# Optimization experiments

Hardware: AMD Instinct MI355X
Metric: run time of the kernel (lower is better)

The kernel has to match this reference:

```python
import jax, jax.numpy as jnp
import numpy as np

D = 256; H = 4; HD = 64; WBAND = 64; KLOC = 8; EMAK = 256
SUMDECAY = 0.9; STATEDECAY = 0.9; STEP = 0.5


def _dwconv(x, kern, pad):
    # x: (B,T,D), kern: (D,1,K) cross-correlation taps, causal left pad
    lhs = jnp.transpose(x, (0, 2, 1))
    out = jax.lax.conv_general_dilated(
        lhs, kern, (1,), [(pad, 0)],
        dimension_numbers=('NCH', 'OIH', 'NCH'),
        feature_group_count=x.shape[-1])
    return jnp.transpose(out, (0, 2, 1))


def _ln(x, g, b):
    m = jnp.mean(x, -1, keepdims=True)
    v = jnp.var(x, -1, keepdims=True)
    return (x - m) * jax.lax.rsqrt(v + 1e-5) * g + b


def _lin(x, w, b):
    return jnp.dot(x, w.T) + b


def _forward(parallel_repr, sequential_state, trajectory_summary, conv_w, conv_b,
             qkv_w, qkv_b, mo_w, mo_b, fg_w, fg_b, gkv_w, gkv_b, go_w, go_b,
             comb_w, comb_b, ffn1_w, ffn1_b, ffn2_w, ffn2_b, tr1_w, tr1_b,
             tr2_w, tr2_b, p2s_w, p2s_b, s2p_w, s2p_b,
             ln1_g, ln1_b, ln2_g, ln2_b, ln3_g, ln3_b, ln4_g, ln4_b):
    B, T, _ = parallel_repr.shape
    # Tier 1: local depthwise causal conv (window 8); torch pads both sides then slices [:T] == causal left pad
    local_history = _dwconv(parallel_repr, conv_w, KLOC - 1) + conv_b
    # Tier 2: banded causal attention (keep j in [i-63, i])
    qkv = _lin(parallel_repr, qkv_w, qkv_b).reshape(B, T, 3, H, HD)
    qkv = jnp.transpose(qkv, (2, 0, 3, 1, 4))  # (3,B,H,T,HD)
    q, k, v = qkv[0], qkv[1], qkv[2]
    idx = jnp.arange(T)
    band = (idx[:, None] >= idx[None, :]) & (idx[None, :] > idx[:, None] - WBAND)
    scores = jnp.einsum('bhqd,bhkd->bhqk', q, k) / jnp.sqrt(jnp.float32(HD))
    attn = jax.nn.softmax(jnp.where(band, scores, -1e9), -1)
    med = jnp.einsum('bhqk,bhkd->bhqd', attn, v)
    med = jnp.transpose(med, (0, 2, 1, 3)).reshape(B, T, D)
    med = _lin(med, mo_w, mo_b)
    fg = jax.nn.sigmoid(_lin(jnp.concatenate([parallel_repr, med], -1), fg_w, fg_b))
    medium_out = med * fg
    # Tier 3: causal cumulative (linear-attention style) global concepts
    gkv = _lin(parallel_repr, gkv_w, gkv_b)
    gk, gv = jnp.split(gkv, 2, -1)
    gk = jax.nn.elu(gk) + 1.0
    concepts = jnp.cumsum(gk * gv, 1) / (jnp.cumsum(gk, 1) + 1e-5)
    global_out = _lin(concepts, go_w, go_b)
    combined = _lin(jnp.concatenate([local_history, medium_out, global_out], -1), comb_w, comb_b)
    pr = _ln(parallel_repr + combined, ln1_g, ln1_b)
    # EMA summary via 256-tap causal depthwise conv: w[i] = (1-d)*d^i
    kE = min(T, EMAK)
    taps = (1.0 - SUMDECAY) * SUMDECAY ** jnp.arange(kE, dtype=jnp.float32)
    kern = jnp.broadcast_to(taps[::-1][None, None, :], (D, 1, kE))
    global_summary = _dwconv(pr, kern, kE - 1)
    guidance = _lin(pr, p2s_w, p2s_b)
    cs = jnp.concatenate([pr + 0.3 * guidance, global_summary], -1)
    deltas = jnp.tanh(_lin(jax.nn.gelu(_lin(cs, tr1_w, tr1_b), approximate=False), tr2_w, tr2_b))
    scaled = deltas * STEP
    # state accumulation via conv trick: acc[t] = sum_i d^i * delta[t-i]
    staps = STATEDECAY ** jnp.arange(kE, dtype=jnp.float32)
    skern = jnp.broadcast_to(staps[::-1][None, None, :], (D, 1, kE))
    acc = _dwconv(scaled, skern, kE - 1)
    dpow = STATEDECAY ** jnp.arange(1, T + 1, dtype=jnp.float32)
    pre_ln = sequential_state[:, None, :] * dpow[None, :, None] + acc
    states = _ln(pre_ln, ln3_g, ln3_b)
    seq_g = _lin(states, s2p_w, s2p_b)
    ffn = _lin(jax.nn.gelu(_lin(pr + 0.3 * seq_g, ffn1_w, ffn1_b), approximate=False), ffn2_w, ffn2_b)
    pr_out = _ln(pr + ffn, ln2_g, ln2_b)
    final_state = _ln(states[:, -1, :], ln4_g, ln4_b)
    final_traj = global_summary[:, -1, :]
    return pr_out, final_state, final_traj


def setup_inputs():
    key = jax.random.key(0)
    ks = jax.random.split(key, 20)
    B, T = 4, 2048
    s = 0.02
    def w(i, shape):
        return jax.random.normal(ks[i], shape, jnp.float32) * s
    return {
        'parallel_repr': jax.random.normal(ks[0], (B, T, D), jnp.float32),
        'sequential_state': jax.random.normal(ks[1], (B, D), jnp.float32),
        'trajectory_summary': jax.random.normal(ks[2], (B, D), jnp.float32),
        'conv_w': w(3, (D, 1, KLOC)), 'conv_b': jnp.zeros((D,)),
        'qkv_w': w(4, (3 * D, D)), 'qkv_b': jnp.zeros((3 * D,)),
        'mo_w': w(5, (D, D)), 'mo_b': jnp.zeros((D,)),
        'fg_w': w(6, (D, 2 * D)), 'fg_b': jnp.zeros((D,)),
        'gkv_w': w(7, (2 * D, D)), 'gkv_b': jnp.zeros((2 * D,)),
        'go_w': w(8, (D, D)), 'go_b': jnp.zeros((D,)),
        'comb_w': w(9, (D, 3 * D)), 'comb_b': jnp.zeros((D,)),
        'ffn1_w': w(10, (4 * D, D)), 'ffn1_b': jnp.zeros((4 * D,)),
        'ffn2_w': w(11, (D, 4 * D)), 'ffn2_b': jnp.zeros((D,)),
        'tr1_w': w(12, (2 * D, 2 * D)), 'tr1_b': jnp.zeros((2 * D,)),
        'tr2_w': w(13, (D, 2 * D)), 'tr2_b': jnp.zeros((D,)),
        'p2s_w': w(14, (D, D)), 'p2s_b': jnp.zeros((D,)),
        's2p_w': w(15, (D, D)), 's2p_b': jnp.zeros((D,)),
        'ln1_g': jnp.ones((D,)), 'ln1_b': jnp.zeros((D,)),
        'ln2_g': jnp.ones((D,)), 'ln2_b': jnp.zeros((D,)),
        'ln3_g': jnp.ones((D,)), 'ln3_b': jnp.zeros((D,)),
        'ln4_g': jnp.ones((D,)), 'ln4_b': jnp.zeros((D,)),
    }


def reference(parallel_repr, sequential_state, trajectory_summary, conv_w, conv_b,
              qkv_w, qkv_b, mo_w, mo_b, fg_w, fg_b, gkv_w, gkv_b, go_w, go_b,
              comb_w, comb_b, ffn1_w, ffn1_b, ffn2_w, ffn2_b, tr1_w, tr1_b,
              tr2_w, tr2_b, p2s_w, p2s_b, s2p_w, s2p_b,
              ln1_g, ln1_b, ln2_g, ln2_b, ln3_g, ln3_b, ln4_g, ln4_b):
    return _forward(parallel_repr, sequential_state, trajectory_summary, conv_w, conv_b,
                    qkv_w, qkv_b, mo_w, mo_b, fg_w, fg_b, gkv_w, gkv_b, go_w, go_b,
                    comb_w, comb_b, ffn1_w, ffn1_b, ffn2_w, ffn2_b, tr1_w, tr1_b,
                    tr2_w, tr2_b, p2s_w, p2s_b, s2p_w, s2p_b,
                    ln1_g, ln1_b, ln2_g, ln2_b, ln3_g, ln3_b, ln4_g, ln4_b)
```

## Files before the change

kernel.cpp:

```cpp
#include <hip/hip_runtime.h>
#include <hip/hip_bf16.h>
#include <math.h>

#define D_  256
#define T_  2048
#define B_  4
#define M_  (B_*T_)
#define H_  4
#define HD_ 64

#define NC_ 64
#define LCH (T_/NC_)

enum { OP_NONE=0, OP_SIGMUL=1, OP_ADDAUX=2, OP_AXPBY=3, OP_GELU=4, OP_TANHHALF=5 };

typedef unsigned short u16;
typedef short short8 __attribute__((ext_vector_type(8)));
typedef float f32x4  __attribute__((ext_vector_type(4)));

__device__ __forceinline__ float gelu_f(float x){ return 0.5f*x*(1.0f+erff(x*0.70710678118654752f)); }
__device__ __forceinline__ float sigmoid_f(float x){ return 1.0f/(1.0f+expf(-x)); }

__device__ __forceinline__ unsigned pk2(float a, float b){
    __hip_bfloat162 h = __float22bfloat162_rn(make_float2(a,b));
    union { __hip_bfloat162 h; unsigned u; } c; c.h = h; return c.u;
}
__device__ __forceinline__ float bfu(u16 u){ return __uint_as_float(((unsigned)u)<<16); }
__device__ __forceinline__ u16 bf1(float x){ return (u16)(pk2(x,x)&0xffffu); }

#define OFF_QKV   0u
#define OFF_MO    327680u
#define OFF_FG    393216u
#define OFF_GO    524288u
#define OFF_COMB  589824u
#define OFF_FFN1  786432u
#define OFF_FFN2  1048576u
#define OFF_TR1   1310720u
#define OFF_TR2   1572864u
#define OFF_P2S   1703936u
#define OFF_S2P   1769472u
#define NWELEM    1835008u
#define NXELEM    2097152u

__global__ __launch_bounds__(256) void cvt_k(
    const float* __restrict__ qkv_w, const float* __restrict__ gkv_w,
    const float* __restrict__ qkv_b, const float* __restrict__ gkv_b,
    const float* __restrict__ mo_w,  const float* __restrict__ fg_w,
    const float* __restrict__ go_w,  const float* __restrict__ comb_w,
    const float* __restrict__ ffn1_w,const float* __restrict__ ffn2_w,
    const float* __restrict__ tr1_w, const float* __restrict__ tr2_w,
    const float* __restrict__ p2s_w, const float* __restrict__ s2p_w,
    const float* __restrict__ X,
    u16* __restrict__ Wh, u16* __restrict__ Xh, float* __restrict__ bq)
{
    size_t i = ((size_t)blockIdx.x*256 + threadIdx.x)*4;
    if (i < NWELEM){
        const float* s; size_t base;
        if      (i < OFF_MO)  { s=(i<196608)?qkv_w:gkv_w; base=(i<196608)?0:196608; }
        else if (i < OFF_FG)  { s=mo_w;   base=OFF_MO; }
        else if (i < OFF_GO)  { s=fg_w;   base=OFF_FG; }
        else if (i < OFF_COMB){ s=go_w;   base=OFF_GO; }
        else if (i < OFF_FFN1){ s=comb_w; base=OFF_COMB; }
        else if (i < OFF_FFN2){ s=ffn1_w; base=OFF_FFN1; }
        else if (i < OFF_TR1) { s=ffn2_w; base=OFF_FFN2; }
        else if (i < OFF_TR2) { s=tr1_w;  base=OFF_TR1; }
        else if (i < OFF_P2S) { s=tr2_w;  base=OFF_TR2; }
        else if (i < OFF_S2P) { s=p2s_w;  base=OFF_P2S; }
        else                  { s=s2p_w;  base=OFF_S2P; }
        float4 v = *(const float4*)(s + (i-base));
        *(uint2*)(Wh + i) = (uint2){ pk2(v.x,v.y), pk2(v.z,v.w) };
    } else if (i < NWELEM + NXELEM){
        size_t j = i - NWELEM;
        float4 v = *(const float4*)(X + j);
        *(uint2*)(Xh + j) = (uint2){ pk2(v.x,v.y), pk2(v.z,v.w) };
    } else if (i < NWELEM + NXELEM + 1280){
        size_t j = i - (NWELEM + NXELEM);
        #pragma unroll
        for (int k=0;k<4;++k){
            size_t e = j + k;
            bq[e] = (e < 768) ? qkv_b[e] : gkv_b[e-768];
        }
    }
}

__global__ __launch_bounds__(512) void gemm_k(
    const u16* __restrict__ A0, const u16* __restrict__ W0, int ldw0, int K0,
    const u16* __restrict__ A1, const u16* __restrict__ W1, int ldw1, int K1,
    const u16* __restrict__ A2, const u16* __restrict__ W2, int ldw2, int K2,
    const float* __restrict__ bias, const void* __restrict__ aux, int aux_bf16,
    void* __restrict__ C, int ldc, int c_bf16, int op, int ncol)
{
    __shared__ u16 As[128*64];
    __shared__ u16 Ws[64*64];

    const int q8   = gridDim.x >> 3;
    const int lid  = (blockIdx.x & 7)*q8 + (blockIdx.x >> 3);
    const int brow = lid / ncol;
    const int bcol = lid - brow*ncol;
    const int row0 = brow*128, col0 = bcol*64;

    const int tid  = threadIdx.x;
    const int lane = tid & 63, wid = tid >> 6;
    const int wm = (wid >> 1)*32, wn = (wid & 1)*32;
    const int l15 = lane & 15, l4 = lane >> 4;
    const int rowA = tid >> 2;
    const int scA  = (tid & 3) * 8;
    const int rowW = tid >> 3;
    const int scW  = (tid & 7) * 8;

    f32x4 acc[2][2];
    #pragma unroll
    for (int i=0;i<2;++i)
        #pragma unroll
        for (int j=0;j<2;++j) acc[i][j] = (f32x4){0.f,0.f,0.f,0.f};

    uint4 ra0, ra1, rw0;

    auto loadtile = [&](const u16* A, const u16* W, int ldw, int K, int kb){
        const u16* ga = A + (size_t)(row0+rowA)*K + kb + scA;
        ra0 = *(const uint4*)ga;
        ra1 = *(const uint4*)(ga + 32);
        rw0 = *(const uint4*)(W + (size_t)(col0+rowW)*ldw + kb + scW);
    };
    auto storetile = [&](){
        const int sw = (rowA&7)<<3;
        *(uint4*)&As[(rowA*64 + scA) ^ sw]      = ra0;
        *(uint4*)&As[(rowA*64 + scA + 32) ^ sw] = ra1;
        *(uint4*)&Ws[(rowW*64 + scW) ^ ((rowW&7)<<3)] = rw0;
    };
    auto mfma_tile = [&](){
        #pragma unroll
        for (int ks=0;ks<2;++ks){
            const int koff = ks*32 + l4*8;
            short8 af[2], bf[2];
            #pragma unroll
            for (int f=0;f<2;++f){
                const int ar = wm + f*16 + l15;
                af[f] = *(const short8*)&As[(ar*64 + koff) ^ ((ar&7)<<3)];
                const int brn = wn + f*16 + l15;
                bf[f] = *(const short8*)&Ws[(brn*64 + koff) ^ ((brn&7)<<3)];
            }
            #pragma unroll
            for (int fm=0;fm<2;++fm)
                #pragma unroll
                for (int fn=0;fn<2;++fn)
                    acc[fm][fn] = __builtin_amdgcn_mfma_f32_16x16x32_bf16(
                        af[fm], bf[fn], acc[fm][fn], 0, 0, 0);
        }
    };

    const u16* Ac = A0; const u16* Wc = W0; int ldwc = ldw0, Kc = K0, kb = 0;
    loadtile(Ac, Wc, ldwc, Kc, 0);
    while (true){
        __syncthreads();
        storetile();
        __syncthreads();
        int nkb = kb + 64;
        const u16* nA = Ac; const u16* nW = Wc; int nld = ldwc, nK = Kc;
        bool have_next = true;
        if (nkb >= Kc){
            if (Ac == A0 && A1){ nA = A1; nW = W1; nld = ldw1; nK = K1; nkb = 0; }
            else if (Ac == A1 && A2){ nA = A2; nW = W2; nld = ldw2; nK = K2; nkb = 0; }
            else have_next = false;
        }
        if (have_next) loadtile(nA, nW, nld, nK, nkb);
        mfma_tile();
        if (!have_next) break;
        Ac = nA; Wc = nW; ldwc = nld; Kc = nK; kb = nkb;
    }

    #pragma unroll
    for (int fn=0;fn<2;++fn){
        const int n = col0 + wn + fn*16 + l15;
        const float bv = bias[n];
        #pragma unroll
        for (int fm=0;fm<2;++fm){
            #pragma unroll
            for (int j=0;j<4;++j){
                const int m = row0 + wm + fm*16 + l4*4 + j;
                float v = acc[fm][fn][j] + bv;
                if (op==OP_GELU)          v = gelu_f(v);
                else if (op==OP_TANHHALF) v = 0.5f*tanhf(v);
                else if (op!=OP_NONE){
                    const size_t ai = (size_t)m*D_ + n;
                    const float a = aux_bf16 ? bfu(((const u16*)aux)[ai])
                                             : ((const float*)aux)[ai];
                    if (op==OP_SIGMUL)      v = a*sigmoid_f(v);
                    else if (op==OP_ADDAUX) v = v + a;
                    else                    v = a + 0.3f*v;
                }
                if (c_bf16) ((u16*)C)[(size_t)m*ldc + n] = bf1(v);
                else        ((float*)C)[(size_t)m*ldc + n] = v;
            }
        }
    }
}

__global__ __launch_bounds__(256) void conv_k(const u16* __restrict__ Xh,
    const float* __restrict__ w, const float* __restrict__ bias, u16* __restrict__ out)
{
    int idx = blockIdx.x*256 + threadIdx.x;
    int d4 = (idx & 63) * 4;
    int bt = idx >> 6;
    int t = bt & (T_-1);
    float a0 = bias[d4], a1 = bias[d4+1], a2 = bias[d4+2], a3 = bias[d4+3];
    const u16* xp = Xh + (size_t)bt*D_ + d4;
    #pragma unroll
    for (int j=0;j<8;++j){
        int tt = t - 7 + j;
        if (tt >= 0){
            uint2 v = *(const uint2*)(xp + (size_t)(j-7)*D_);
            a0 += bfu((u16)(v.x & 0xffff))      * w[(d4+0)*8 + j];
            a1 += bfu((u16)(v.x >> 16))         * w[(d4+1)*8 + j];
            a2 += bfu((u16)(v.y & 0xffff))      * w[(d4+2)*8 + j];
            a3 += bfu((u16)(v.y >> 16))         * w[(d4+3)*8 + j];
        }
    }
    *(uint2*)(out + (size_t)bt*D_ + d4) = (uint2){ pk2(a0,a1), pk2(a2,a3) };
}

__global__ __launch_bounds__(256) void attn_k(const u16* __restrict__ QKVG,
    u16* __restrict__ MED)
{
    __shared__ u16 Kl[128*64];
    __shared__ u16 Ql[64*64];
    __shared__ u16 Vl[64*128];
    const int b = blockIdx.z, h = blockIdx.y;
    const int t0 = blockIdx.x * 64;
    const int kb0 = t0 - 64;
    const int tid = threadIdx.x;

    {
        const int r0 = tid >> 3, c8 = (tid & 7) * 8;
        #pragma unroll
        for (int rep=0;rep<4;++rep){
            const int r = r0 + rep*32;
            const int kg = kb0 + r;
            uint4 pk = {0,0,0,0}, pv = {0,0,0,0};
            if (kg >= 0){
                const u16* gp = QKVG + ((size_t)(b*T_ + kg))*1280 + h*HD_ + c8;
                pk = *(const uint4*)(gp + 256);
                pv = *(const uint4*)(gp + 512);
            }
            *(uint4*)&Kl[(r*64 + c8) ^ ((r&7)<<3)] = pk;
            const u16* pvu = (const u16*)&pv;
            #pragma unroll
            for (int j=0;j<8;++j){
                const int d = c8 + j;
                Vl[(d*128 + r) ^ ((d&15)<<3)] = pvu[j];
            }
        }
        #pragma unroll
        for (int rep=0;rep<2;++rep){
            const int r = r0 + rep*32;
            uint4 pq = *(const uint4*)(QKVG + ((size_t)(b*T_ + t0 + r))*1280 + h*HD_ + c8);
            *(uint4*)&Ql[(r*64 + c8) ^ ((r&7)<<3)] = pq;
        }
    }
    __syncthreads();

    const int lane = tid & 63, w = tid >> 6;
    const int l15 = lane & 15, l4 = lane >> 4;

    short8 bq[2];
    {
        const int qr = w*16 + l15;
        bq[0] = *(const short8*)&Ql[(qr*64 +      l4*8) ^ ((qr&7)<<3)];
        bq[1] = *(const short8*)&Ql[(qr*64 + 32 + l4*8) ^ ((qr&7)<<3)];
    }

    f32x4 s[8];
    #pragma unroll
    for (int kf=0;kf<8;++kf){
        const int kr = kf*16 + l15;
        short8 a0 = *(const short8*)&Kl[(kr*64 +      l4*8) ^ ((kr&7)<<3)];
        short8 a1 = *(const short8*)&Kl[(kr*64 + 32 + l4*8) ^ ((kr&7)<<3)];
        f32x4 acc = (f32x4){0.f,0.f,0.f,0.f};
        acc = __builtin_amdgcn_mfma_f32_16x16x32_bf16(a0, bq[0], acc, 0,0,0);
        acc = __builtin_amdgcn_mfma_f32_16x16x32_bf16(a1, bq[1], acc, 0,0,0);
        s[kf] = acc;
    }

    const int qg = t0 + w*16 + l15;
    float m = -1e30f;
    #pragma unroll
    for (int kf=0;kf<8;++kf){
        #pragma unroll
        for (int j=0;j<4;++j){
            const int kg = kb0 + kf*16 + l4*4 + j;
            const int diff = qg - kg;
            const float v = (kg >= 0 && diff >= 0 && diff < 64) ? s[kf][j]*0.125f : -1e30f;
            s[kf][j] = v;
            m = fmaxf(m, v);
        }
    }
    m = fmaxf(m, __shfl_xor(m,16));
    m = fmaxf(m, __shfl_xor(m,32));
    float lsum = 0.f;
    unsigned lo[8], hi[8];
    #pragma unroll
    for (int kf=0;kf<8;++kf){
        const float p0 = expf(s[kf][0]-m), p1 = expf(s[kf][1]-m);
        const float p2 = expf(s[kf][2]-m), p3 = expf(s[kf][3]-m);
        lsum += (p0+p1)+(p2+p3);
        lo[kf] = pk2(p0,p1);
        hi[kf] = pk2(p2,p3);
    }
    lsum += __shfl_xor(lsum,16);
    lsum += __shfl_xor(lsum,32);
    const float inv = 1.f/lsum;

    f32x4 o[4];
    #pragma unroll
    for (int df=0;df<4;++df) o[df] = (f32x4){0.f,0.f,0.f,0.f};
    const int baseLane = l15 + ((l4&1)<<5);
    const bool hiHalf = (l4>>1) != 0;
    #pragma unroll
    for (int kb=0;kb<4;++kb){
        const int x0 = __shfl((int)lo[2*kb],   baseLane);
        const int x1 = __shfl((int)hi[2*kb],   baseLane);
        const int x2 = __shfl((int)lo[2*kb],   baseLane+16);
        const int x3 = __shfl((int)hi[2*kb],   baseLane+16);
        const int y0 = __shfl((int)lo[2*kb+1], baseLane);
        const int y1 = __shfl((int)hi[2*kb+1], baseLane);
        const int y2 = __shfl((int)lo[2*kb+1], baseLane+16);
        const int y3 = __shfl((int)hi[2*kb+1], baseLane+16);
        int4 afi;
        afi.x = hiHalf ? y0 : x0;
        afi.y = hiHalf ? y1 : x1;
        afi.z = hiHalf ? y2 : x2;
        afi.w = hiHalf ? y3 : x3;
        union { int4 i; short8 s; } cv; cv.i = afi;
        #pragma unroll
        for (int df=0;df<4;++df){
            const int vr = df*16 + l15;
            short8 bv = *(const short8*)&Vl[(vr*128 + kb*32 + l4*8) ^ ((vr&15)<<3)];
            o[df] = __builtin_amdgcn_mfma_f32_16x16x32_bf16(cv.s, bv, o[df], 0,0,0);
        }
    }

    #pragma unroll
    for (int j=0;j<4;++j){
        const float invj = __shfl(inv, l4*4 + j);
        const int mrow = b*T_ + t0 + w*16 + l4*4 + j;
        u16* op = MED + (size_t)mrow*D_ + h*HD_ + l15;
        #pragma unroll
        for (int df=0;df<4;++df)
            op[df*16] = bf1(o[df][j] * invj);
    }
}

__global__ __launch_bounds__(256) void scan1_p1(const u16* __restrict__ QKVG,
    float* __restrict__ CA, float* __restrict__ CC)
{
    const int d = threadIdx.x, c = blockIdx.x, b = blockIdx.y;
    const u16* base = QKVG + ((size_t)(b*T_ + c*LCH))*1280;
    float sgk=0.f, sgkv=0.f;
    for (int t=0;t<LCH;++t){
        float gk = bfu(base[(size_t)t*1280 + 768 + d]);
        gk = gk > 0.f ? gk + 1.f : expf(gk);
        float gv = bfu(base[(size_t)t*1280 + 1024 + d]);
        sgk += gk; sgkv += gk*gv;
    }
    CA[((size_t)b*NC_ + c)*D_ + d] = sgk;
    CC[((size_t)b*NC_ + c)*D_ + d] = sgkv;
}

__global__ __launch_bounds__(256) void scan1_p3(const u16* __restrict__ QKVG,
    const float* __restrict__ CA, const float* __restrict__ CC, u16* __restrict__ CONC)
{
    const int d = threadIdx.x, c = blockIdx.x, b = blockIdx.y;
    float sgk = 0.f, sgkv = 0.f;
    for (int cc=0; cc<c; ++cc){
        sgk  += CA[((size_t)b*NC_ + cc)*D_ + d];
        sgkv += CC[((size_t)b*NC_ + cc)*D_ + d];
    }
    const u16* base = QKVG + ((size_t)(b*T_ + c*LCH))*1280;
    u16* out = CONC + ((size_t)(b*T_ + c*LCH))*D_ + d;
    for (int t=0;t<LCH;++t){
        float gk = bfu(base[(size_t)t*1280 + 768 + d]);
        gk = gk > 0.f ? gk + 1.f : expf(gk);
        float gv = bfu(base[(size_t)t*1280 + 1024 + d]);
        sgk += gk; sgkv += gk*gv;
        out[(size_t)t*D_] = bf1(sgkv / (sgk + 1e-5f));
    }
}

__global__ __launch_bounds__(256) void ema_p1h(const u16* __restrict__ X,
    float* __restrict__ CARRY, float alpha)
{
    const int d = threadIdx.x, c = blockIdx.x, b = blockIdx.y;
    const u16* xp = X + ((size_t)(b*T_ + c*LCH))*D_ + d;
    float g = 0.f;
    for (int t=0;t<LCH;++t) g = 0.9f*g + alpha*bfu(xp[(size_t)t*D_]);
    CARRY[((size_t)b*NC_ + c)*D_ + d] = g;
}

__global__ __launch_bounds__(256) void ema_p3h(const u16* __restrict__ X,
    const float* __restrict__ CARRY, u16* __restrict__ OUT, float alpha,
    float* __restrict__ traj)
{
    const int d = threadIdx.x, c = blockIdx.x, b = blockIdx.y;
    const float dL = powf(0.9f, (float)LCH);
    float g = 0.f;
    for (int cc=0; cc<c; ++cc) g = CARRY[((size_t)b*NC_ + cc)*D_ + d] + dL*g;
    const u16* xp = X + ((size_t)(b*T_ + c*LCH))*D_ + d;
    u16* op = OUT + ((size_t)(b*T_ + c*LCH))*D_ + d;
    for (int t=0;t<LCH;++t){
        g = 0.9f*g + alpha*bfu(xp[(size_t)t*D_]);
        op[(size_t)t*D_] = bf1(g);
    }
    if (c == NC_-1) traj[b*D_ + d] = g;
}

__global__ __launch_bounds__(256) void ema_p3_state_h(const u16* __restrict__ X,
    const float* __restrict__ CARRY, const float* __restrict__ SEQ, float* __restrict__ OUT)
{
    const int d = threadIdx.x, c = blockIdx.x, b = blockIdx.y;
    const float dL = powf(0.9f, (float)LCH);
    float a = 0.f;
    for (int cc=0; cc<c; ++cc) a = CARRY[((size_t)b*NC_ + cc)*D_ + d] + dL*a;
    const float ss = SEQ[b*D_ + d];
    float dp = powf(0.9f, (float)(c*LCH + 1));
    const u16* xp = X + ((size_t)(b*T_ + c*LCH))*D_ + d;
    float* op = OUT + ((size_t)(b*T_ + c*LCH))*D_ + d;
    for (int t=0;t<LCH;++t){
        a = 0.9f*a + bfu(xp[(size_t)t*D_]);
        op[(size_t)t*D_] = fmaf(ss, dp, a);
        dp *= 0.9f;
    }
}

__global__ __launch_bounds__(256) void ln_k(const float* __restrict__ in,
    const float* __restrict__ g, const float* __restrict__ b,
    float* __restrict__ out, u16* __restrict__ out2)
{
    int row  = blockIdx.x*4 + (threadIdx.x>>6);
    int lane = threadIdx.x & 63;
    const float* ip = in + (size_t)row*D_ + lane*4;
    float4 x = *(const float4*)ip;
    float s  = x.x+x.y+x.z+x.w;
    float s2 = x.x*x.x + x.y*x.y + x.z*x.z + x.w*x.w;
    #pragma unroll
    for (int o=1;o<64;o<<=1){ s += __shfl_xor(s,o); s2 += __shfl_xor(s2,o); }
    float mean = s * (1.f/256.f);
    float var  = s2 * (1.f/256.f) - mean*mean;
    float rs = rsqrtf(var + 1e-5f);
    int db = lane*4;
    float4 r;
    r.x=(x.x-mean)*rs*g[db+0]+b[db+0];
    r.y=(x.y-mean)*rs*g[db+1]+b[db+1];
    r.z=(x.z-mean)*rs*g[db+2]+b[db+2];
    r.w=(x.w-mean)*rs*g[db+3]+b[db+3];
    if (out)
        *(float4*)(out + (size_t)row*D_ + db) = r;
    if (out2)
        *(uint2*)(out2 + (size_t)row*D_ + db) = (uint2){ pk2(r.x,r.y), pk2(r.z,r.w) };
}

__global__ __launch_bounds__(256) void ln3_k(const float* __restrict__ in,
    const float* __restrict__ g3, const float* __restrict__ b3, u16* __restrict__ states,
    const float* __restrict__ g4, const float* __restrict__ b4, float* __restrict__ fsout)
{
    int row  = blockIdx.x*4 + (threadIdx.x>>6);
    int lane = threadIdx.x & 63;
    const float* ip = in + (size_t)row*D_ + lane*4;
    float4 x = *(const float4*)ip;
    float s  = x.x+x.y+x.z+x.w;
    float s2 = x.x*x.x + x.y*x.y + x.z*x.z + x.w*x.w;
    #pragma unroll
    for (int o=1;o<64;o<<=1){ s += __shfl_xor(s,o); s2 += __shfl_xor(s2,o); }
    float mean = s * (1.f/256.f);
    float var  = s2 * (1.f/256.f) - mean*mean;
    float rs = rsqrtf(var + 1e-5f);
    int db = lane*4;
    float4 st;
    st.x=(x.x-mean)*rs*g3[db+0]+b3[db+0];
    st.y=(x.y-mean)*rs*g3[db+1]+b3[db+1];
    st.z=(x.z-mean)*rs*g3[db+2]+b3[db+2];
    st.w=(x.w-mean)*rs*g3[db+3]+b3[db+3];
    *(uint2*)(states + (size_t)row*D_ + db) = (uint2){ pk2(st.x,st.y), pk2(st.z,st.w) };

    if ((row & (T_-1)) == T_-1){
        float u  = st.x+st.y+st.z+st.w;
        float u2 = st.x*st.x + st.y*st.y + st.z*st.z + st.w*st.w;
        #pragma unroll
        for (int o=1;o<64;o<<=1){ u += __shfl_xor(u,o); u2 += __shfl_xor(u2,o); }
        float m2 = u * (1.f/256.f);
        float v2 = u2 * (1.f/256.f) - m2*m2;
        float r2 = rsqrtf(v2 + 1e-5f);
        float4 fs;
        fs.x=(st.x-m2)*r2*g4[db+0]+b4[db+0];
        fs.y=(st.y-m2)*r2*g4[db+1]+b4[db+1];
        fs.z=(st.z-m2)*r2*g4[db+2]+b4[db+2];
        fs.w=(st.w-m2)*r2*g4[db+3]+b4[db+3];
        *(float4*)(fsout + (size_t)(row>>11)*D_ + db) = fs;
    }
}

extern "C" void kernel_launch(void* const* d_in, const int* in_sizes, int n_in,
                              void* d_out, int out_size, void* d_ws, size_t ws_size,
                              hipStream_t stream)
{
    const float* X     = (const float*)d_in[0];
    const float* SEQ   = (const float*)d_in[1];
    const float* conv_w= (const float*)d_in[3];
    const float* conv_b= (const float*)d_in[4];
    const float* qkv_w = (const float*)d_in[5];
    const float* qkv_b = (const float*)d_in[6];
    const float* mo_w  = (const float*)d_in[7];
    const float* mo_b  = (const float*)d_in[8];
    const float* fg_w  = (const float*)d_in[9];
    const float* fg_b  = (const float*)d_in[10];
    const float* gkv_w = (const float*)d_in[11];
    const float* gkv_b = (const float*)d_in[12];
    const float* go_w  = (const float*)d_in[13];
    const float* go_b  = (const float*)d_in[14];
    const float* comb_w= (const float*)d_in[15];
    const float* comb_b= (const float*)d_in[16];
    const float* ffn1_w= (const float*)d_in[17];
    const float* ffn1_b= (const float*)d_in[18];
    const float* ffn2_w= (const float*)d_in[19];
    const float* ffn2_b= (const float*)d_in[20];
    const float* tr1_w = (const float*)d_in[21];
    const float* tr1_b = (const float*)d_in[22];
    const float* tr2_w = (const float*)d_in[23];
    const float* tr2_b = (const float*)d_in[24];
    const float* p2s_w = (const float*)d_in[25];
    const float* p2s_b = (const float*)d_in[26];
    const float* s2p_w = (const float*)d_in[27];
    const float* s2p_b = (const float*)d_in[28];
    const float* ln1_g = (const float*)d_in[29];
    const float* ln1_b = (const float*)d_in[30];
    const float* ln2_g = (const float*)d_in[31];
    const float* ln2_b = (const float*)d_in[32];
    const float* ln3_g = (const float*)d_in[33];
    const float* ln3_b = (const float*)d_in[34];
    const float* ln4_g = (const float*)d_in[35];
    const float* ln4_b = (const float*)d_in[36];

    char* p = (char*)d_ws;
    auto alloc = [&](size_t bytes)->char*{ char* r = p; p += (bytes + 255) & ~(size_t)255; return r; };

    u16*   QKVG = (u16*)  alloc((size_t)M_*1280*2);
    u16*   Wh   = (u16*)  alloc((size_t)NWELEM*2);
    float* bq   = (float*)alloc(1280*4);
    u16*   Xh   = (u16*)  alloc((size_t)M_*256*2);
    u16*   MED  = (u16*)  alloc((size_t)M_*256*2);
    u16*   MED2 = (u16*)  alloc((size_t)M_*256*2);
    u16*   LH   = (u16*)  alloc((size_t)M_*256*2);
    u16*   CONC = (u16*)  alloc((size_t)M_*256*2);
    u16*   GOUT = (u16*)  alloc((size_t)M_*256*2);
    u16*   MOUT = (u16*)  alloc((size_t)M_*256*2);
    float* PRE1 = (float*)alloc((size_t)M_*256*4);
    u16*   PRh  = (u16*)  alloc((size_t)M_*256*2);
    u16*   GSUM = (u16*)  alloc((size_t)M_*256*2);
    u16*   CS1  = (u16*)  alloc((size_t)M_*256*2);
    u16*   H1   = (u16*)  alloc((size_t)M_*512*2);
    u16*   SCALEDh=(u16*) alloc((size_t)M_*256*2);
    float* PRE3 = (float*)alloc((size_t)M_*256*4);
    u16*   STATESh=(u16*) alloc((size_t)M_*256*2);
    u16*   FFNIN= (u16*)  alloc((size_t)M_*256*2);
    u16*   H2   = (u16*)  alloc((size_t)M_*1024*2);
    float* PRE2 = (float*)alloc((size_t)M_*256*4);
    float* CAR0 = (float*)alloc((size_t)B_*NC_*D_*4);
    float* CAR1 = (float*)alloc((size_t)B_*NC_*D_*4);

    float* out_pr = (float*)d_out;
    float* out_fs = out_pr + (size_t)M_*256;
    float* out_tj = out_fs + B_*256;

    const dim3 blk256(256), blk512(512);
    const dim3 scan_grid(NC_, B_);
    const int NRg = M_/128;

    cvt_k<<<dim3(3842), blk256, 0, stream>>>(
        qkv_w, gkv_w, qkv_b, gkv_b, mo_w, fg_w, go_w, comb_w,
        ffn1_w, ffn2_w, tr1_w, tr2_w, p2s_w, s2p_w, X, Wh, Xh, bq);
    gemm_k<<<dim3(NRg*20), blk512, 0, stream>>>(
        Xh, Wh+OFF_QKV, 256, 256,  nullptr,nullptr,0,0,  nullptr,nullptr,0,0,
        bq, nullptr, 0, QKVG, 1280, 1, OP_NONE, 20);
    conv_k<<<dim3(M_*D_/1024), blk256, 0, stream>>>(Xh, conv_w, conv_b, LH);
    attn_k<<<dim3(T_/64, H_, B_), blk256, 0, stream>>>(QKVG, MED);
    gemm_k<<<dim3(NRg*4), blk512, 0, stream>>>(
        MED, Wh+OFF_MO, 256, 256,  nullptr,nullptr,0,0,  nullptr,nullptr,0,0,
        mo_b, nullptr, 0, MED2, 256, 1, OP_NONE, 4);
    scan1_p1<<<scan_grid, blk256, 0, stream>>>(QKVG, CAR0, CAR1);
    scan1_p3<<<scan_grid, blk256, 0, stream>>>(QKVG, CAR0, CAR1, CONC);
    gemm_k<<<dim3(NRg*4), blk512, 0, stream>>>(
        CONC, Wh+OFF_GO, 256, 256,  nullptr,nullptr,0,0,  nullptr,nullptr,0,0,
        go_b, nullptr, 0, GOUT, 256, 1, OP_NONE, 4);
    gemm_k<<<dim3(NRg*4), blk512, 0, stream>>>(
        Xh, Wh+OFF_FG, 512, 256,  MED2, Wh+OFF_FG+256, 512, 256,  nullptr,nullptr,0,0,
        fg_b, MED2, 1, MOUT, 256, 1, OP_SIGMUL, 4);
    gemm_k<<<dim3(NRg*4), blk512, 0, stream>>>(
        LH, Wh+OFF_COMB, 768, 256,  MOUT, Wh+OFF_COMB+256, 768, 256,  GOUT, Wh+OFF_COMB+512, 768, 256,
        comb_b, X, 0, PRE1, 256, 0, OP_ADDAUX, 4);
    ln_k<<<dim3(M_/4), blk256, 0, stream>>>(PRE1, ln1_g, ln1_b, nullptr, PRh);
    ema_p1h<<<scan_grid, blk256, 0, stream>>>(PRh, CAR0, 0.1f);
    ema_p3h<<<scan_grid, blk256, 0, stream>>>(PRh, CAR0, GSUM, 0.1f, out_tj);
    gemm_k<<<dim3(NRg*4), blk512, 0, stream>>>(
        PRh, Wh+OFF_P2S, 256, 256,  nullptr,nullptr,0,0,  nullptr,nullptr,0,0,
        p2s_b, PRh, 1, CS1, 256, 1, OP_AXPBY, 4);
    gemm_k<<<dim3(NRg*8), blk512, 0, stream>>>(
        CS1, Wh+OFF_TR1, 512, 256,  GSUM, Wh+OFF_TR1+256, 512, 256,  nullptr,nullptr,0,0,
        tr1_b, nullptr, 0, H1, 512, 1, OP_GELU, 8);
    gemm_k<<<dim3(NRg*4), blk512, 0, stream>>>(
        H1, Wh+OFF_TR2, 512, 512,  nullptr,nullptr,0,0,  nullptr,nullptr,0,0,
        tr2_b, nullptr, 0, SCALEDh, 256, 1, OP_TANHHALF, 4);
    ema_p1h<<<scan_grid, blk256, 0, stream>>>(SCALEDh, CAR0, 1.0f);
    ema_p3_state_h<<<scan_grid, blk256, 0, stream>>>(SCALEDh, CAR0, SEQ, PRE3);
    ln3_k<<<dim3(M_/4), blk256, 0, stream>>>(PRE3, ln3_g, ln3_b, STATESh, ln4_g, ln4_b, out_fs);
    gemm_k<<<dim3(NRg*4), blk512, 0, stream>>>(
        STATESh, Wh+OFF_S2P, 256, 256,  nullptr,nullptr,0,0,  nullptr,nullptr,0,0,
        s2p_b, PRh, 1, FFNIN, 256, 1, OP_AXPBY, 4);
    gemm_k<<<dim3(NRg*16), blk512, 0, stream>>>(
        FFNIN, Wh+OFF_FFN1, 256, 256,  nullptr,nullptr,0,0,  nullptr,nullptr,0,0,
        ffn1_b, nullptr, 0, H2, 1024, 1, OP_GELU, 16);
    gemm_k<<<dim3(NRg*4), blk512, 0, stream>>>(
        H2, Wh+OFF_FFN2, 1024, 1024,  nullptr,nullptr,0,0,  nullptr,nullptr,0,0,
        ffn2_b, PRh, 1, PRE2, 256, 0, OP_ADDAUX, 4);
    ln_k<<<dim3(M_/4), blk256, 0, stream>>>(PRE2, ln2_g, ln2_b, out_pr, nullptr);
}
```

Before: 259.8 us.

## Fuse conv into convert, LN1 with EMA carry, EMA with LN3; bf16 pre-LN buffers

Merges the depthwise conv into the weight-conversion launch, reading X in fp32. Fuses LayerNorm1 with the per-chunk EMA carry computation, and the state EMA with LayerNorm3/LN4 through shared memory. Stores the pre-LN GEMM outputs in bf16 instead of fp32. Together this removes several launches and fp32 intermediate round trips through memory. The cost is extra rounding before the LayerNorms, and LN1 and LN3 now run on only 256 blocks, each a mostly serial per-chunk loop.

```diff
diff --git a/kernel.cpp b/kernel.cpp
--- a/kernel.cpp
+++ b/kernel.cpp
@@ -41,8 +41,10 @@
 #define OFF_S2P   1769472u
 #define NWELEM    1835008u
 #define NXELEM    2097152u
-
-__global__ __launch_bounds__(256) void cvt_k(
+#define CVT_BLKS  3842u
+#define CONV_BLKS 2048u
+
+__global__ __launch_bounds__(256) void cvt_conv_k(
     const float* __restrict__ qkv_w, const float* __restrict__ gkv_w,
     const float* __restrict__ qkv_b, const float* __restrict__ gkv_b,
     const float* __restrict__ mo_w,  const float* __restrict__ fg_w,
@@ -51,8 +53,31 @@
     const float* __restrict__ tr1_w, const float* __restrict__ tr2_w,
     const float* __restrict__ p2s_w, const float* __restrict__ s2p_w,
     const float* __restrict__ X,
-    u16* __restrict__ Wh, u16* __restrict__ Xh, float* __restrict__ bq)
-{
+    const float* __restrict__ conv_w, const float* __restrict__ conv_b,
+    u16* __restrict__ Wh, u16* __restrict__ Xh, float* __restrict__ bq,
+    u16* __restrict__ LH)
+{
+    if (blockIdx.x >= CVT_BLKS){
+        int idx = (blockIdx.x - CVT_BLKS)*256 + threadIdx.x;
+        int d4 = (idx & 63) * 4;
+        int bt = idx >> 6;
+        int t = bt & (T_-1);
+        float a0 = conv_b[d4], a1 = conv_b[d4+1], a2 = conv_b[d4+2], a3 = conv_b[d4+3];
+        const float* xp = X + (size_t)bt*D_ + d4;
+        #pragma unroll
+        for (int j=0;j<8;++j){
+            int tt = t - 7 + j;
+            if (tt >= 0){
+                float4 v = *(const float4*)(xp + (size_t)(j-7)*D_);
+                a0 += v.x * conv_w[(d4+0)*8 + j];
+                a1 += v.y * conv_w[(d4+1)*8 + j];
+                a2 += v.z * conv_w[(d4+2)*8 + j];
+                a3 += v.w * conv_w[(d4+3)*8 + j];
+            }
+        }
+        *(uint2*)(LH + (size_t)bt*D_ + d4) = (uint2){ pk2(a0,a1), pk2(a2,a3) };
+        return;
+    }
     size_t i = ((size_t)blockIdx.x*256 + threadIdx.x)*4;
     if (i < NWELEM){
         const float* s; size_t base;
@@ -196,29 +221,6 @@
     }
 }
 
-__global__ __launch_bounds__(256) void conv_k(const u16* __restrict__ Xh,
-    const float* __restrict__ w, const float* __restrict__ bias, u16* __restrict__ out)
-{
-    int idx = blockIdx.x*256 + threadIdx.x;
-    int d4 = (idx & 63) * 4;
-    int bt = idx >> 6;
-    int t = bt & (T_-1);
-    float a0 = bias[d4], a1 = bias[d4+1], a2 = bias[d4+2], a3 = bias[d4+3];
-    const u16* xp = Xh + (size_t)bt*D_ + d4;
-    #pragma unroll
-    for (int j=0;j<8;++j){
-        int tt = t - 7 + j;
-        if (tt >= 0){
-            uint2 v = *(const uint2*)(xp + (size_t)(j-7)*D_);
-            a0 += bfu((u16)(v.x & 0xffff))      * w[(d4+0)*8 + j];
-            a1 += bfu((u16)(v.x >> 16))         * w[(d4+1)*8 + j];
-            a2 += bfu((u16)(v.y & 0xffff))      * w[(d4+2)*8 + j];
-            a3 += bfu((u16)(v.y >> 16))         * w[(d4+3)*8 + j];
-        }
-    }
-    *(uint2*)(out + (size_t)bt*D_ + d4) = (uint2){ pk2(a0,a1), pk2(a2,a3) };
-}
-
 __global__ __launch_bounds__(256) void attn_k(const u16* __restrict__ QKVG,
     u16* __restrict__ MED)
 {
@@ -413,34 +415,115 @@
     if (c == NC_-1) traj[b*D_ + d] = g;
 }
 
-__global__ __launch_bounds__(256) void ema_p3_state_h(const u16* __restrict__ X,
-    const float* __restrict__ CARRY, const float* __restrict__ SEQ, float* __restrict__ OUT)
-{
-    const int d = threadIdx.x, c = blockIdx.x, b = blockIdx.y;
+__global__ __launch_bounds__(256) void ln1ema_k(const u16* __restrict__ in,
+    const float* __restrict__ g, const float* __restrict__ b,
+    u16* __restrict__ out, float* __restrict__ CARRY)
+{
+    __shared__ float wacc[4][256];
+    const int c = blockIdx.x, bb = blockIdx.y;
+    const int w = threadIdx.x >> 6, lane = threadIdx.x & 63;
+    const int db = lane*4;
+    const int row0 = bb*T_ + c*LCH;
+    float acc0=0.f, acc1=0.f, acc2=0.f, acc3=0.f;
+    #pragma unroll
+    for (int it=0; it<8; ++it){
+        const int r = it*4 + w;
+        uint2 u = *(const uint2*)(in + (size_t)(row0 + r)*D_ + db);
+        float x0=bfu((u16)(u.x&0xffff)), x1=bfu((u16)(u.x>>16));
+        float x2=bfu((u16)(u.y&0xffff)), x3=bfu((u16)(u.y>>16));
+        float s  = x0+x1+x2+x3;
+        float s2 = x0*x0+x1*x1+x2*x2+x3*x3;
+        #pragma unroll
+        for (int o=1;o<64;o<<=1){ s += __shfl_xor(s,o); s2 += __shfl_xor(s2,o); }
+        float mean = s*(1.f/256.f);
+        float var  = s2*(1.f/256.f) - mean*mean;
+        float rs = rsqrtf(var + 1e-5f);
+        float y0=(x0-mean)*rs*g[db+0]+b[db+0];
+        float y1=(x1-mean)*rs*g[db+1]+b[db+1];
+        float y2=(x2-mean)*rs*g[db+2]+b[db+2];
+        float y3=(x3-mean)*rs*g[db+3]+b[db+3];
+        *(uint2*)(out + (size_t)(row0+r)*D_ + db) = (uint2){ pk2(y0,y1), pk2(y2,y3) };
+        const float wt = 0.1f*powf(0.9f, (float)(31-r));
+        acc0 += wt*y0; acc1 += wt*y1; acc2 += wt*y2; acc3 += wt*y3;
+    }
+    wacc[w][db+0]=acc0; wacc[w][db+1]=acc1; wacc[w][db+2]=acc2; wacc[w][db+3]=acc3;
+    __syncthreads();
+    const int d = threadIdx.x;
+    CARRY[((size_t)bb*NC_ + c)*D_ + d] =
+        wacc[0][d] + wacc[1][d] + wacc[2][d] + wacc[3][d];
+}
+
+__global__ __launch_bounds__(256) void ema_ln3_k(const u16* __restrict__ X,
+    const float* __restrict__ CARRY, const float* __restrict__ SEQ,
+    const float* __restrict__ g3, const float* __restrict__ b3, u16* __restrict__ states,
+    const float* __restrict__ g4, const float* __restrict__ b4, float* __restrict__ fsout)
+{
+    __shared__ float vals[LCH][256];
+    __shared__ float mv[LCH][2];
+    __shared__ float st4[256];
+    __shared__ float red[8];
+    const int d = threadIdx.x, c = blockIdx.x, bb = blockIdx.y;
     const float dL = powf(0.9f, (float)LCH);
     float a = 0.f;
-    for (int cc=0; cc<c; ++cc) a = CARRY[((size_t)b*NC_ + cc)*D_ + d] + dL*a;
-    const float ss = SEQ[b*D_ + d];
+    for (int cc=0; cc<c; ++cc) a = CARRY[((size_t)bb*NC_ + cc)*D_ + d] + dL*a;
+    const float ss = SEQ[bb*D_ + d];
     float dp = powf(0.9f, (float)(c*LCH + 1));
-    const u16* xp = X + ((size_t)(b*T_ + c*LCH))*D_ + d;
-    float* op = OUT + ((size_t)(b*T_ + c*LCH))*D_ + d;
+    const u16* xp = X + ((size_t)(bb*T_ + c*LCH))*D_ + d;
     for (int t=0;t<LCH;++t){
         a = 0.9f*a + bfu(xp[(size_t)t*D_]);
-        op[(size_t)t*D_] = fmaf(ss, dp, a);
+        vals[t][d] = fmaf(ss, dp, a);
         dp *= 0.9f;
     }
-}
-
-__global__ __launch_bounds__(256) void ln_k(const float* __restrict__ in,
-    const float* __restrict__ g, const float* __restrict__ b,
-    float* __restrict__ out, u16* __restrict__ out2)
+    __syncthreads();
+    {
+        const int r = threadIdx.x >> 3, seg = threadIdx.x & 7;
+        float s=0.f, s2=0.f;
+        #pragma unroll
+        for (int j=0;j<32;++j){ float v = vals[r][seg*32+j]; s += v; s2 += v*v; }
+        s += __shfl_xor(s,1); s2 += __shfl_xor(s2,1);
+        s += __shfl_xor(s,2); s2 += __shfl_xor(s2,2);
+        s += __shfl_xor(s,4); s2 += __shfl_xor(s2,4);
+        if (seg == 0){
+            float mean = s*(1.f/256.f);
+            float var  = s2*(1.f/256.f) - mean*mean;
+            mv[r][0] = mean; mv[r][1] = rsqrtf(var + 1e-5f);
+        }
+    }
+    __syncthreads();
+    const float gd = g3[d], bd = b3[d];
+    const bool isLast = (c == NC_-1);
+    u16* sp = states + ((size_t)(bb*T_ + c*LCH))*D_ + d;
+    for (int t=0;t<LCH;++t){
+        float st = (vals[t][d] - mv[t][0])*mv[t][1]*gd + bd;
+        sp[(size_t)t*D_] = bf1(st);
+        if (isLast && t == LCH-1) st4[d] = st;
+    }
+    if (isLast){
+        __syncthreads();
+        float v = st4[d];
+        float s = v, s2 = v*v;
+        #pragma unroll
+        for (int o=1;o<64;o<<=1){ s += __shfl_xor(s,o); s2 += __shfl_xor(s2,o); }
+        if ((threadIdx.x & 63) == 0){ red[threadIdx.x>>6] = s; red[4+(threadIdx.x>>6)] = s2; }
+        __syncthreads();
+        float S  = red[0]+red[1]+red[2]+red[3];
+        float S2 = red[4]+red[5]+red[6]+red[7];
+        float m2 = S*(1.f/256.f);
+        float r2 = rsqrtf(S2*(1.f/256.f) - m2*m2 + 1e-5f);
+        fsout[bb*D_ + d] = (st4[d]-m2)*r2*g4[d] + b4[d];
+    }
+}
+
+__global__ __launch_bounds__(256) void ln2h_k(const u16* __restrict__ in,
+    const float* __restrict__ g, const float* __restrict__ b, float* __restrict__ out)
 {
     int row  = blockIdx.x*4 + (threadIdx.x>>6);
     int lane = threadIdx.x & 63;
-    const float* ip = in + (size_t)row*D_ + lane*4;
-    float4 x = *(const float4*)ip;
-    float s  = x.x+x.y+x.z+x.w;
-    float s2 = x.x*x.x + x.y*x.y + x.z*x.z + x.w*x.w;
+    uint2 u = *(const uint2*)(in + (size_t)row*D_ + lane*4);
+    float x0=bfu((u16)(u.x&0xffff)), x1=bfu((u16)(u.x>>16));
+    float x2=bfu((u16)(u.y&0xffff)), x3=bfu((u16)(u.y>>16));
+    float s  = x0+x1+x2+x3;
+    float s2 = x0*x0+x1*x1+x2*x2+x3*x3;
     #pragma unroll
     for (int o=1;o<64;o<<=1){ s += __shfl_xor(s,o); s2 += __shfl_xor(s2,o); }
     float mean = s * (1.f/256.f);
@@ -448,54 +531,11 @@
     float rs = rsqrtf(var + 1e-5f);
     int db = lane*4;
     float4 r;
-    r.x=(x.x-mean)*rs*g[db+0]+b[db+0];
-    r.y=(x.y-mean)*rs*g[db+1]+b[db+1];
-    r.z=(x.z-mean)*rs*g[db+2]+b[db+2];
-    r.w=(x.w-mean)*rs*g[db+3]+b[db+3];
-    if (out)
-        *(float4*)(out + (size_t)row*D_ + db) = r;
-    if (out2)
-        *(uint2*)(out2 + (size_t)row*D_ + db) = (uint2){ pk2(r.x,r.y), pk2(r.z,r.w) };
-}
-
-__global__ __launch_bounds__(256) void ln3_k(const float* __restrict__ in,
-    const float* __restrict__ g3, const float* __restrict__ b3, u16* __restrict__ states,
-    const float* __restrict__ g4, const float* __restrict__ b4, float* __restrict__ fsout)
-{
-    int row  = blockIdx.x*4 + (threadIdx.x>>6);
-    int lane = threadIdx.x & 63;
-    const float* ip = in + (size_t)row*D_ + lane*4;
-    float4 x = *(const float4*)ip;
-    float s  = x.x+x.y+x.z+x.w;
-    float s2 = x.x*x.x + x.y*x.y + x.z*x.z + x.w*x.w;
-    #pragma unroll
-    for (int o=1;o<64;o<<=1){ s += __shfl_xor(s,o); s2 += __shfl_xor(s2,o); }
-    float mean = s * (1.f/256.f);
-    float var  = s2 * (1.f/256.f) - mean*mean;
-    float rs = rsqrtf(var + 1e-5f);
-    int db = lane*4;
-    float4 st;
-    st.x=(x.x-mean)*rs*g3[db+0]+b3[db+0];
-    st.y=(x.y-mean)*rs*g3[db+1]+b3[db+1];
-    st.z=(x.z-mean)*rs*g3[db+2]+b3[db+2];
-    st.w=(x.w-mean)*rs*g3[db+3]+b3[db+3];
-    *(uint2*)(states + (size_t)row*D_ + db) = (uint2){ pk2(st.x,st.y), pk2(st.z,st.w) };
-
-    if ((row & (T_-1)) == T_-1){
-        float u  = st.x+st.y+st.z+st.w;
-        float u2 = st.x*st.x + st.y*st.y + st.z*st.z + st.w*st.w;
-        #pragma unroll
-        for (int o=1;o<64;o<<=1){ u += __shfl_xor(u,o); u2 += __shfl_xor(u2,o); }
-        float m2 = u * (1.f/256.f);
-        float v2 = u2 * (1.f/256.f) - m2*m2;
-        float r2 = rsqrtf(v2 + 1e-5f);
-        float4 fs;
-        fs.x=(st.x-m2)*r2*g4[db+0]+b4[db+0];
-        fs.y=(st.y-m2)*r2*g4[db+1]+b4[db+1];
-        fs.z=(st.z-m2)*r2*g4[db+2]+b4[db+2];
-        fs.w=(st.w-m2)*r2*g4[db+3]+b4[db+3];
-        *(float4*)(fsout + (size_t)(row>>11)*D_ + db) = fs;
-    }
+    r.x=(x0-mean)*rs*g[db+0]+b[db+0];
+    r.y=(x1-mean)*rs*g[db+1]+b[db+1];
+    r.z=(x2-mean)*rs*g[db+2]+b[db+2];
+    r.w=(x3-mean)*rs*g[db+3]+b[db+3];
+    *(float4*)(out + (size_t)row*D_ + db) = r;
 }
 
 extern "C" void kernel_launch(void* const* d_in, const int* in_sizes, int n_in,
@@ -552,17 +592,16 @@
     u16*   CONC = (u16*)  alloc((size_t)M_*256*2);
     u16*   GOUT = (u16*)  alloc((size_t)M_*256*2);
     u16*   MOUT = (u16*)  alloc((size_t)M_*256*2);
-    float* PRE1 = (float*)alloc((size_t)M_*256*4);
+    u16*   PRE1h= (u16*)  alloc((size_t)M_*256*2);
     u16*   PRh  = (u16*)  alloc((size_t)M_*256*2);
     u16*   GSUM = (u16*)  alloc((size_t)M_*256*2);
     u16*   CS1  = (u16*)  alloc((size_t)M_*256*2);
     u16*   H1   = (u16*)  alloc((size_t)M_*512*2);
     u16*   SCALEDh=(u16*) alloc((size_t)M_*256*2);
-    float* PRE3 = (float*)alloc((size_t)M_*256*4);
     u16*   STATESh=(u16*) alloc((size_t)M_*256*2);
     u16*   FFNIN= (u16*)  alloc((size_t)M_*256*2);
     u16*   H2   = (u16*)  alloc((size_t)M_*1024*2);
-    float* PRE2 = (float*)alloc((size_t)M_*256*4);
+    u16*   PRE2h= (u16*)  alloc((size_t)M_*256*2);
     float* CAR0 = (float*)alloc((size_t)B_*NC_*D_*4);
     float* CAR1 = (float*)alloc((size_t)B_*NC_*D_*4);
 
@@ -574,13 +613,13 @@
     const dim3 scan_grid(NC_, B_);
     const int NRg = M_/128;
 
-    cvt_k<<<dim3(3842), blk256, 0, stream>>>(
+    cvt_conv_k<<<dim3(CVT_BLKS + CONV_BLKS), blk256, 0, stream>>>(
         qkv_w, gkv_w, qkv_b, gkv_b, mo_w, fg_w, go_w, comb_w,
-        ffn1_w, ffn2_w, tr1_w, tr2_w, p2s_w, s2p_w, X, Wh, Xh, bq);
+        ffn1_w, ffn2_w, tr1_w, tr2_w, p2s_w, s2p_w, X, conv_w, conv_b,
+        Wh, Xh, bq, LH);
     gemm_k<<<dim3(NRg*20), blk512, 0, stream>>>(
         Xh, Wh+OFF_QKV, 256, 256,  nullptr,nullptr,0,0,  nullptr,nullptr,0,0,
         bq, nullptr, 0, QKVG, 1280, 1, OP_NONE, 20);
-    conv_k<<<dim3(M_*D_/1024), blk256, 0, stream>>>(Xh, conv_w, conv_b, LH);
     attn_k<<<dim3(T_/64, H_, B_), blk256, 0, stream>>>(QKVG, MED);
     gemm_k<<<dim3(NRg*4), blk512, 0, stream>>>(
         MED, Wh+OFF_MO, 256, 256,  nullptr,nullptr,0,0,  nullptr,nullptr,0,0,
@@ -595,9 +634,8 @@
         fg_b, MED2, 1, MOUT, 256, 1, OP_SIGMUL, 4);
     gemm_k<<<dim3(NRg*4), blk512, 0, stream>>>(
         LH, Wh+OFF_COMB, 768, 256,  MOUT, Wh+OFF_COMB+256, 768, 256,  GOUT, Wh+OFF_COMB+512, 768, 256,
-        comb_b, X, 0, PRE1, 256, 0, OP_ADDAUX, 4);
-    ln_k<<<dim3(M_/4), blk256, 0, stream>>>(PRE1, ln1_g, ln1_b, nullptr, PRh);
-    ema_p1h<<<scan_grid, blk256, 0, stream>>>(PRh, CAR0, 0.1f);
+        comb_b, X, 0, PRE1h, 256, 1, OP_ADDAUX, 4);
+    ln1ema_k<<<scan_grid, blk256, 0, stream>>>(PRE1h, ln1_g, ln1_b, PRh, CAR0);
     ema_p3h<<<scan_grid, blk256, 0, stream>>>(PRh, CAR0, GSUM, 0.1f, out_tj);
     gemm_k<<<dim3(NRg*4), blk512, 0, stream>>>(
         PRh, Wh+OFF_P2S, 256, 256,  nullptr,nullptr,0,0,  nullptr,nullptr,0,0,
@@ -609,8 +647,8 @@
         H1, Wh+OFF_TR2, 512, 512,  nullptr,nullptr,0,0,  nullptr,nullptr,0,0,
         tr2_b, nullptr, 0, SCALEDh, 256, 1, OP_TANHHALF, 4);
     ema_p1h<<<scan_grid, blk256, 0, stream>>>(SCALEDh, CAR0, 1.0f);
-    ema_p3_state_h<<<scan_grid, blk256, 0, stream>>>(SCALEDh, CAR0, SEQ, PRE3);
-    ln3_k<<<dim3(M_/4), blk256, 0, stream>>>(PRE3, ln3_g, ln3_b, STATESh, ln4_g, ln4_b, out_fs);
+    ema_ln3_k<<<scan_grid, blk256, 0, stream>>>(
+        SCALEDh, CAR0, SEQ, ln3_g, ln3_b, STATESh, ln4_g, ln4_b, out_fs);
     gemm_k<<<dim3(NRg*4), blk512, 0, stream>>>(
         STATESh, Wh+OFF_S2P, 256, 256,  nullptr,nullptr,0,0,  nullptr,nullptr,0,0,
         s2p_b, PRh, 1, FFNIN, 256, 1, OP_AXPBY, 4);
@@ -619,6 +657,6 @@
         ffn1_b, nullptr, 0, H2, 1024, 1, OP_GELU, 16);
     gemm_k<<<dim3(NRg*4), blk512, 0, stream>>>(
         H2, Wh+OFF_FFN2, 1024, 1024,  nullptr,nullptr,0,0,  nullptr,nullptr,0,0,
-        ffn2_b, PRh, 1, PRE2, 256, 0, OP_ADDAUX, 4);
-    ln_k<<<dim3(M_/4), blk256, 0, stream>>>(PRE2, ln2_g, ln2_b, out_pr, nullptr);
-}
+        ffn2_b, PRh, 1, PRE2h, 256, 1, OP_ADDAUX, 4);
+    ln2h_k<<<dim3(M_/4), blk256, 0, stream>>>(PRE2h, ln2_g, ln2_b, out_pr);
+}
```

New measurement: 253.4 us. -2.5%, faster.
